# Kernel optimization log

Hardware: AMD Instinct MI355X
Metric: run time of the kernel (lower is better)

The kernel has to match this reference:

```python
import jax, jax.numpy as jnp
import numpy as np

N, C, D = 200000, 100, 256      # samples, classes, dim_out
M = N // C                       # samples per class (y is sorted, equal counts)
K = int(1000 * 0.1)              # num_overlab = int(args.d * args.overlap_ratio)
ALPHA = 1.0                      # args.alpha


def setup_inputs() -> dict:
    key = jax.random.key(0)
    x = jax.random.normal(key, (N, D), dtype=jnp.float32)
    # sorted, balanced labels: class c occupies rows [c*M, (c+1)*M)
    y = jnp.arange(N, dtype=jnp.int32) // M
    return {"x": x, "y": y}


def reference(x, y):
    # per-class means (faithful to get_centers); y is sorted/balanced so a
    # reshape gives the static per-class grouping used below
    xg = x.reshape(C, M, D)                         # [C, M, D]
    centers = jax.ops.segment_sum(x, y, num_segments=C) / M  # [C, D]

    # full center-to-sample L2 distances via ||c||^2 + ||x||^2 - 2 c.x
    x2 = jnp.sum(xg * xg, axis=-1)                  # [C2, M]
    c2 = jnp.sum(centers * centers, axis=-1)        # [C1]
    cx = jnp.einsum('cd,gmd->cgm', centers, xg)     # [C1, C2, M]
    dist = jnp.sqrt(jnp.maximum(c2[:, None, None] + x2[None, :, :] - 2.0 * cx, 0.0))

    # positive: K largest distances from each center to its own samples
    pos = jnp.einsum('iim->im', dist)               # diagonal blocks [C, M]
    pos_mean = jax.lax.top_k(pos, K)[0].mean(axis=1)            # [C]

    # negative: K smallest distances from center c1 to samples of class c2
    neg_mean = (-jax.lax.top_k(-dist, K)[0]).mean(axis=-1)      # [C1, C2]

    lo = jnp.maximum(ALPHA + pos_mean[:, None] - neg_mean, 0.0)  # [C1, C2]
    mask = 1.0 - jnp.eye(C, dtype=lo.dtype)         # skip class_type2 == class_type1
    loss = jnp.sum(lo * mask) / ((C + 1) * (C / 2))
    return loss.reshape(1)
```

## Files before the change

### kernel.cpp

```cpp
#include <hip/hip_runtime.h>
#include <hip/hip_fp16.h>
#include <math.h>

#define N_S 200000
#define C_CLS 100
#define D_DIM 256
#define M_PER 2000
#define K_SEL 100
#define EP_STRIDE 136

typedef __attribute__((ext_vector_type(8))) short short8;
typedef __attribute__((ext_vector_type(4))) float float4v;

__device__ __forceinline__ unsigned int f2bf(float f){
    unsigned int u = __float_as_uint(f);
    u += 0x7FFFu + ((u >> 16) & 1u);
    return u >> 16;
}

__global__ __launch_bounds__(256) void k_sums(const float* __restrict__ x,
                                              float* __restrict__ partial){
    int c = blockIdx.x, s = blockIdx.y;
    int t = threadIdx.x, w = t >> 6, ch = t & 63;
    int rbase = c * M_PER + s * 125;
    float a0 = 0.f, a1 = 0.f, a2 = 0.f, a3 = 0.f;
    for (int i = 0; i < 32; ++i){
        int rl = w + 4 * i;
        if (rl < 125){
            float4v v = *(const float4v*)(x + (size_t)(rbase + rl) * D_DIM + ch * 4);
            a0 += v[0]; a1 += v[1]; a2 += v[2]; a3 += v[3];
        }
    }
    float4v o = {a0, a1, a2, a3};
    *(float4v*)(partial + ((size_t)((c * 16 + s) * 4 + w)) * D_DIM + ch * 4) = o;
}

__global__ __launch_bounds__(256) void k_centers(const float* __restrict__ partial,
                                                 unsigned short* __restrict__ cbf,
                                                 float* __restrict__ c2){
    int c = blockIdx.x, d = threadIdx.x;
    const float* pp = partial + (size_t)c * 64 * D_DIM + d;
    float v = 0.f;
    #pragma unroll
    for (int s = 0; s < 64; ++s) v += pp[(size_t)s * D_DIM];
    v *= (1.0f / (float)M_PER);
    cbf[c * D_DIM + d] = (unsigned short)f2bf(v);
    float sq = v * v;
    #pragma unroll
    for (int m = 1; m < 64; m <<= 1) sq += __shfl_xor(sq, m);
    __shared__ float sred[4];
    if ((threadIdx.x & 63) == 0) sred[threadIdx.x >> 6] = sq;
    __syncthreads();
    if (threadIdx.x == 0) c2[c] = (sred[0] + sred[1]) + (sred[2] + sred[3]);
}

__global__ __launch_bounds__(256, 3) void k_gemm(const float* __restrict__ x,
                                                 const unsigned short* __restrict__ cbf,
                                                 const float* __restrict__ c2,
                                                 _Float16* __restrict__ dist2h){
    __shared__ unsigned short s_cent[C_CLS * 264];
    __shared__ float s_c2[C_CLS];
    int tid = threadIdx.x;
    {
        const uint4* g = (const uint4*)cbf;
        #pragma unroll
        for (int i = 0; i < 13; ++i){
            int q = i * 256 + tid;
            if (q < 3200){
                uint4 v = g[q];
                int row = q >> 5;
                int col = q & 31;
                *(uint4*)((char*)s_cent + row * 528 + col * 16) = v;
            }
        }
        if (tid < C_CLS) s_c2[tid] = c2[tid];
    }
    __syncthreads();

    int wid = tid >> 6, lane = tid & 63, lo = lane & 15, hi = lane >> 4;
    int sbase = blockIdx.x * 128 + wid * 32;
    int j0 = sbase + lo, j1 = sbase + 16 + lo;
    int jr0 = j0 < N_S ? j0 : N_S - 1;
    int jr1 = j1 < N_S ? j1 : N_S - 1;

    float4v acc[7][2];
    #pragma unroll
    for (int a = 0; a < 7; ++a){
        #pragma unroll
        for (int b = 0; b < 2; ++b) acc[a][b] = (float4v){0.f, 0.f, 0.f, 0.f};
    }
    float px2_0 = 0.f, px2_1 = 0.f;

    const float* xr0 = x + (size_t)jr0 * D_DIM + hi * 8;
    const float* xr1 = x + (size_t)jr1 * D_DIM + hi * 8;
    for (int ks = 0; ks < 8; ++ks){
        int k0 = ks * 32;
        float4v v0 = *(const float4v*)(xr0 + k0);
        float4v v1 = *(const float4v*)(xr0 + k0 + 4);
        float4v w0 = *(const float4v*)(xr1 + k0);
        float4v w1 = *(const float4v*)(xr1 + k0 + 4);
        px2_0 += v0[0]*v0[0] + v0[1]*v0[1] + v0[2]*v0[2] + v0[3]*v0[3]
               + v1[0]*v1[0] + v1[1]*v1[1] + v1[2]*v1[2] + v1[3]*v1[3];
        px2_1 += w0[0]*w0[0] + w0[1]*w0[1] + w0[2]*w0[2] + w0[3]*w0[3]
               + w1[0]*w1[0] + w1[1]*w1[1] + w1[2]*w1[2] + w1[3]*w1[3];
        short8 bfr0, bfr1;
        bfr0[0]=(short)f2bf(v0[0]); bfr0[1]=(short)f2bf(v0[1]); bfr0[2]=(short)f2bf(v0[2]); bfr0[3]=(short)f2bf(v0[3]);
        bfr0[4]=(short)f2bf(v1[0]); bfr0[5]=(short)f2bf(v1[1]); bfr0[6]=(short)f2bf(v1[2]); bfr0[7]=(short)f2bf(v1[3]);
        bfr1[0]=(short)f2bf(w0[0]); bfr1[1]=(short)f2bf(w0[1]); bfr1[2]=(short)f2bf(w0[2]); bfr1[3]=(short)f2bf(w0[3]);
        bfr1[4]=(short)f2bf(w1[0]); bfr1[5]=(short)f2bf(w1[1]); bfr1[6]=(short)f2bf(w1[2]); bfr1[7]=(short)f2bf(w1[3]);
        #pragma unroll
        for (int cf = 0; cf < 7; ++cf){
            short8 afr = *(const short8*)((const char*)s_cent + (cf*16 + lo) * 528 + (k0 + hi*8) * 2);
            acc[cf][0] = __builtin_amdgcn_mfma_f32_16x16x32_bf16(afr, bfr0, acc[cf][0], 0, 0, 0);
            acc[cf][1] = __builtin_amdgcn_mfma_f32_16x16x32_bf16(afr, bfr1, acc[cf][1], 0, 0, 0);
        }
    }

    px2_0 += __shfl_xor(px2_0, 16); px2_0 += __shfl_xor(px2_0, 32);
    px2_1 += __shfl_xor(px2_1, 16); px2_1 += __shfl_xor(px2_1, 32);

    __syncthreads();
    _Float16* ep = (_Float16*)s_cent;
    #pragma unroll
    for (int sf = 0; sf < 2; ++sf){
        float x2 = sf ? px2_1 : px2_0;
        int lj = wid * 32 + sf * 16 + lo;
        #pragma unroll
        for (int cf = 0; cf < 7; ++cf){
            #pragma unroll
            for (int r = 0; r < 4; ++r){
                int c1 = cf * 16 + hi * 4 + r;
                if (c1 < C_CLS){
                    float d2 = s_c2[c1] + x2 - 2.0f * acc[cf][sf][r];
                    ep[c1 * EP_STRIDE + lj] = (_Float16)fmaxf(d2, 0.f);
                }
            }
        }
    }
    __syncthreads();

    int blockbase = blockIdx.x * 128;
    int vj = N_S - blockbase; vj = vj > 128 ? 128 : vj;
    for (int q = tid; q < C_CLS * 16; q += 256){
        int row = q >> 4, st = (q & 15) * 8;
        if (st < vj){
            uint4 v = *(const uint4*)(ep + row * EP_STRIDE + st);
            *(uint4*)(dist2h + (size_t)row * N_S + blockbase + st) = v;
        }
    }
}

__global__ __launch_bounds__(256) void k_select(const _Float16* __restrict__ dist2h,
                                                float* __restrict__ pos_mean,
                                                float* __restrict__ neg_mean){
    int lane = threadIdx.x & 63;
    int pair = blockIdx.x * 4 + (threadIdx.x >> 6);
    int c1 = pair / 100, c2 = pair - c1 * 100;
    bool diag = (c1 == c2);
    const uint4* base =
        (const uint4*)(dist2h + (size_t)c1 * N_S + (size_t)c2 * M_PER);

    unsigned pk[16];
    int kmin = 0x10000, kmax = 0;
    #pragma unroll
    for (int i = 0; i < 4; ++i){
        int q = i * 64 + lane;
        uint4 v;
        if (q < 250){
            v = base[q];
            if (diag){ v.x = ~v.x; v.y = ~v.y; v.z = ~v.z; v.w = ~v.w; }
            unsigned wds[4] = {v.x, v.y, v.z, v.w};
            #pragma unroll
            for (int j = 0; j < 4; ++j){
                int a = (int)(wds[j] & 0xFFFFu);
                int b = (int)(wds[j] >> 16);
                kmin = a < kmin ? a : kmin;  kmin = b < kmin ? b : kmin;
                kmax = a > kmax ? a : kmax;  kmax = b > kmax ? b : kmax;
            }
        } else {
            v.x = v.y = v.z = v.w = 0xFFFFFFFFu;
        }
        pk[i*4 + 0] = v.x; pk[i*4 + 1] = v.y; pk[i*4 + 2] = v.z; pk[i*4 + 3] = v.w;
    }
    #pragma unroll
    for (int m = 1; m < 64; m <<= 1){
        int a = __shfl_xor(kmin, m); kmin = a < kmin ? a : kmin;
        int b = __shfl_xor(kmax, m); kmax = b > kmax ? b : kmax;
    }

    int lo = kmin, hi = kmax;
    while (lo < hi){
        int mid = (lo + hi) >> 1;
        int c = 0;
        #pragma unroll
        for (int i = 0; i < 16; ++i){
            c += (int)__popcll(__ballot((int)(pk[i] & 0xFFFFu) <= mid));
            c += (int)__popcll(__ballot((int)(pk[i] >> 16)     <= mid));
        }
        if (c >= K_SEL) hi = mid; else lo = mid + 1;
    }
    int t = lo;

    float sb = 0.f;
    int nb = 0;
    #pragma unroll
    for (int i = 0; i < 16; ++i){
        int ka = (int)(pk[i] & 0xFFFFu);
        int kb = (int)(pk[i] >> 16);
        if (ka < t){
            unsigned short u = (unsigned short)(diag ? (0xFFFF - ka) : ka);
            sb += sqrtf(__half2float(__ushort_as_half(u)));
        }
        if (kb < t){
            unsigned short u = (unsigned short)(diag ? (0xFFFF - kb) : kb);
            sb += sqrtf(__half2float(__ushort_as_half(u)));
        }
        nb += (int)__popcll(__ballot(ka < t));
        nb += (int)__popcll(__ballot(kb < t));
    }
    #pragma unroll
    for (int m = 1; m < 64; m <<= 1) sb += __shfl_xor(sb, m);

    if (lane == 0){
        unsigned short ut = (unsigned short)(diag ? (0xFFFF - t) : t);
        float tval = sqrtf(__half2float(__ushort_as_half(ut)));
        int need = K_SEL - nb;
        float mean = (sb + (float)need * tval) * (1.0f / (float)K_SEL);
        if (diag) pos_mean[c1] = mean; else neg_mean[pair] = mean;
    }
}

__global__ __launch_bounds__(256) void k_loss(const float* __restrict__ pos_mean,
                                              const float* __restrict__ neg_mean,
                                              float* __restrict__ out){
    __shared__ float sred[4];
    int tid = threadIdx.x;
    float s = 0.f;
    for (int idx = tid; idx < C_CLS * C_CLS; idx += 256){
        int c1 = idx / 100, c2 = idx - c1 * 100;
        if (c1 != c2){
            float v = 1.0f + pos_mean[c1] - neg_mean[idx];
            s += fmaxf(v, 0.f);
        }
    }
    #pragma unroll
    for (int m = 1; m < 64; m <<= 1) s += __shfl_xor(s, m);
    if ((tid & 63) == 0) sred[tid >> 6] = s;
    __syncthreads();
    if (tid == 0) out[0] = ((sred[0] + sred[1]) + (sred[2] + sred[3])) * (1.0f / 5050.0f);
}

extern "C" void kernel_launch(void* const* d_in, const int* in_sizes, int n_in,
                              void* d_out, int out_size, void* d_ws, size_t ws_size,
                              hipStream_t stream){
    const float* x = (const float*)d_in[0];
    char* ws = (char*)d_ws;
    _Float16*       dist2h   = (_Float16*)(ws);
    float*          partial  = (float*)(ws + 40000000);
    unsigned short* cbf      = (unsigned short*)(ws + 46553600);
    float*          c2       = (float*)(ws + 46604800);
    float*          pos_mean = (float*)(ws + 46605200);
    float*          neg_mean = (float*)(ws + 46605600);
    float* out = (float*)d_out;

    hipLaunchKernelGGL(k_sums,    dim3(100, 16), dim3(256), 0, stream, x, partial);
    hipLaunchKernelGGL(k_centers, dim3(C_CLS),   dim3(256), 0, stream, partial, cbf, c2);
    hipLaunchKernelGGL(k_gemm,    dim3(1563),    dim3(256), 0, stream, x, cbf, c2, dist2h);
    hipLaunchKernelGGL(k_select,  dim3(2500),    dim3(256), 0, stream, dist2h, pos_mean, neg_mean);
    hipLaunchKernelGGL(k_loss,    dim3(1),       dim3(256), 0, stream, pos_mean, neg_mean, out);
}
```

Before: 126.7 us.

## Fuse all stages into one persistent cooperative kernel with grid syncs

Replaces the five separate launches (sums, centers, gemm, select, loss) with a single cooperative persistent kernel that loops over each stage's tiles and uses grid-wide syncs between stages. This is meant to remove per-launch overhead and the tail gaps between kernels. In exchange, the grid is capped at two blocks per CU, so large stages like the GEMM and selection lose some parallelism. The kernel also makes extra host queries (device attribute, occupancy) on every call, and falls back to the old launches if the cooperative launch fails.

```diff
diff --git a/kernel.cpp b/kernel.cpp
--- a/kernel.cpp
+++ b/kernel.cpp
@@ -1,6 +1,9 @@
 #include <hip/hip_runtime.h>
+#include <hip/hip_cooperative_groups.h>
 #include <hip/hip_fp16.h>
 #include <math.h>
+
+namespace cg = cooperative_groups;
 
 #define N_S 200000
 #define C_CLS 100
@@ -8,6 +11,7 @@
 #define M_PER 2000
 #define K_SEL 100
 #define EP_STRIDE 136
+#define NUM_CU 256
 
 typedef __attribute__((ext_vector_type(8))) short short8;
 typedef __attribute__((ext_vector_type(4))) float float4v;
@@ -16,6 +20,243 @@
     unsigned int u = __float_as_uint(f);
     u += 0x7FFFu + ((u >> 16) & 1u);
     return u >> 16;
+}
+
+__global__ __launch_bounds__(256, 2) void k_fused(const float* __restrict__ x,
+                                                  float* __restrict__ partial,
+                                                  unsigned short* __restrict__ cbf,
+                                                  float* __restrict__ c2,
+                                                  _Float16* __restrict__ dist2h,
+                                                  float* __restrict__ pos_mean,
+                                                  float* __restrict__ neg_mean,
+                                                  float* __restrict__ out){
+    cg::grid_group grid = cg::this_grid();
+    __shared__ unsigned short s_cent[C_CLS * 264];
+    __shared__ float s_c2[C_CLS];
+    __shared__ float sred[4];
+
+    int tid = threadIdx.x;
+    int wid = tid >> 6, lane = tid & 63;
+
+    for (int t = blockIdx.x; t < 1600; t += gridDim.x){
+        int c = t >> 4, s = t & 15;
+        int rbase = c * M_PER + s * 125;
+        float a0 = 0.f, a1 = 0.f, a2 = 0.f, a3 = 0.f;
+        for (int i = 0; i < 32; ++i){
+            int rl = wid + 4 * i;
+            if (rl < 125){
+                float4v v = *(const float4v*)(x + (size_t)(rbase + rl) * D_DIM + lane * 4);
+                a0 += v[0]; a1 += v[1]; a2 += v[2]; a3 += v[3];
+            }
+        }
+        float4v o = {a0, a1, a2, a3};
+        *(float4v*)(partial + ((size_t)((c * 16 + s) * 4 + wid)) * D_DIM + lane * 4) = o;
+    }
+    grid.sync();
+
+    for (int c = blockIdx.x; c < C_CLS; c += gridDim.x){
+        __syncthreads();
+        int d = tid;
+        const float* pp = partial + (size_t)c * 64 * D_DIM + d;
+        float v = 0.f;
+        #pragma unroll
+        for (int s = 0; s < 64; ++s) v += pp[(size_t)s * D_DIM];
+        v *= (1.0f / (float)M_PER);
+        cbf[c * D_DIM + d] = (unsigned short)f2bf(v);
+        float sq = v * v;
+        #pragma unroll
+        for (int m = 1; m < 64; m <<= 1) sq += __shfl_xor(sq, m);
+        if (lane == 0) sred[wid] = sq;
+        __syncthreads();
+        if (tid == 0) c2[c] = (sred[0] + sred[1]) + (sred[2] + sred[3]);
+    }
+    grid.sync();
+
+    for (int t = blockIdx.x; t < 1563; t += gridDim.x){
+        __syncthreads();
+        {
+            const uint4* g = (const uint4*)cbf;
+            #pragma unroll
+            for (int i = 0; i < 13; ++i){
+                int q = i * 256 + tid;
+                if (q < 3200){
+                    uint4 v = g[q];
+                    int row = q >> 5;
+                    int col = q & 31;
+                    *(uint4*)((char*)s_cent + row * 528 + col * 16) = v;
+                }
+            }
+            if (tid < C_CLS) s_c2[tid] = c2[tid];
+        }
+        __syncthreads();
+
+        int lo = lane & 15, hi = lane >> 4;
+        int sbase = t * 128 + wid * 32;
+        int j0 = sbase + lo, j1 = sbase + 16 + lo;
+        int jr0 = j0 < N_S ? j0 : N_S - 1;
+        int jr1 = j1 < N_S ? j1 : N_S - 1;
+
+        float4v acc[7][2];
+        #pragma unroll
+        for (int a = 0; a < 7; ++a){
+            #pragma unroll
+            for (int b = 0; b < 2; ++b) acc[a][b] = (float4v){0.f, 0.f, 0.f, 0.f};
+        }
+        float px2_0 = 0.f, px2_1 = 0.f;
+
+        const float* xr0 = x + (size_t)jr0 * D_DIM + hi * 8;
+        const float* xr1 = x + (size_t)jr1 * D_DIM + hi * 8;
+        for (int ks = 0; ks < 8; ++ks){
+            int k0 = ks * 32;
+            float4v v0 = *(const float4v*)(xr0 + k0);
+            float4v v1 = *(const float4v*)(xr0 + k0 + 4);
+            float4v w0 = *(const float4v*)(xr1 + k0);
+            float4v w1 = *(const float4v*)(xr1 + k0 + 4);
+            px2_0 += v0[0]*v0[0] + v0[1]*v0[1] + v0[2]*v0[2] + v0[3]*v0[3]
+                   + v1[0]*v1[0] + v1[1]*v1[1] + v1[2]*v1[2] + v1[3]*v1[3];
+            px2_1 += w0[0]*w0[0] + w0[1]*w0[1] + w0[2]*w0[2] + w0[3]*w0[3]
+                   + w1[0]*w1[0] + w1[1]*w1[1] + w1[2]*w1[2] + w1[3]*w1[3];
+            short8 bfr0, bfr1;
+            bfr0[0]=(short)f2bf(v0[0]); bfr0[1]=(short)f2bf(v0[1]); bfr0[2]=(short)f2bf(v0[2]); bfr0[3]=(short)f2bf(v0[3]);
+            bfr0[4]=(short)f2bf(v1[0]); bfr0[5]=(short)f2bf(v1[1]); bfr0[6]=(short)f2bf(v1[2]); bfr0[7]=(short)f2bf(v1[3]);
+            bfr1[0]=(short)f2bf(w0[0]); bfr1[1]=(short)f2bf(w0[1]); bfr1[2]=(short)f2bf(w0[2]); bfr1[3]=(short)f2bf(w0[3]);
+            bfr1[4]=(short)f2bf(w1[0]); bfr1[5]=(short)f2bf(w1[1]); bfr1[6]=(short)f2bf(w1[2]); bfr1[7]=(short)f2bf(w1[3]);
+            #pragma unroll
+            for (int cf = 0; cf < 7; ++cf){
+                short8 afr = *(const short8*)((const char*)s_cent + (cf*16 + lo) * 528 + (k0 + hi*8) * 2);
+                acc[cf][0] = __builtin_amdgcn_mfma_f32_16x16x32_bf16(afr, bfr0, acc[cf][0], 0, 0, 0);
+                acc[cf][1] = __builtin_amdgcn_mfma_f32_16x16x32_bf16(afr, bfr1, acc[cf][1], 0, 0, 0);
+            }
+        }
+
+        px2_0 += __shfl_xor(px2_0, 16); px2_0 += __shfl_xor(px2_0, 32);
+        px2_1 += __shfl_xor(px2_1, 16); px2_1 += __shfl_xor(px2_1, 32);
+
+        __syncthreads();
+        _Float16* ep = (_Float16*)s_cent;
+        #pragma unroll
+        for (int sf = 0; sf < 2; ++sf){
+            float x2 = sf ? px2_1 : px2_0;
+            int lj = wid * 32 + sf * 16 + lo;
+            #pragma unroll
+            for (int cf = 0; cf < 7; ++cf){
+                #pragma unroll
+                for (int r = 0; r < 4; ++r){
+                    int c1 = cf * 16 + hi * 4 + r;
+                    if (c1 < C_CLS){
+                        float d2 = s_c2[c1] + x2 - 2.0f * acc[cf][sf][r];
+                        ep[c1 * EP_STRIDE + lj] = (_Float16)fmaxf(d2, 0.f);
+                    }
+                }
+            }
+        }
+        __syncthreads();
+
+        int blockbase = t * 128;
+        int vj = N_S - blockbase; vj = vj > 128 ? 128 : vj;
+        for (int q = tid; q < C_CLS * 16; q += 256){
+            int row = q >> 4, st = (q & 15) * 8;
+            if (st < vj){
+                uint4 v = *(const uint4*)(ep + row * EP_STRIDE + st);
+                *(uint4*)(dist2h + (size_t)row * N_S + blockbase + st) = v;
+            }
+        }
+    }
+    grid.sync();
+
+    for (int task = blockIdx.x; task < 2500; task += gridDim.x){
+        int pair = task * 4 + wid;
+        int c1 = pair / 100, c2i = pair - c1 * 100;
+        bool diag = (c1 == c2i);
+        const uint4* base =
+            (const uint4*)(dist2h + (size_t)c1 * N_S + (size_t)c2i * M_PER);
+
+        unsigned pk[16];
+        int kmin = 0x10000, kmax = 0;
+        #pragma unroll
+        for (int i = 0; i < 4; ++i){
+            int q = i * 64 + lane;
+            uint4 v;
+            if (q < 250){
+                v = base[q];
+                if (diag){ v.x = ~v.x; v.y = ~v.y; v.z = ~v.z; v.w = ~v.w; }
+                unsigned wds[4] = {v.x, v.y, v.z, v.w};
+                #pragma unroll
+                for (int j = 0; j < 4; ++j){
+                    int a = (int)(wds[j] & 0xFFFFu);
+                    int b = (int)(wds[j] >> 16);
+                    kmin = a < kmin ? a : kmin;  kmin = b < kmin ? b : kmin;
+                    kmax = a > kmax ? a : kmax;  kmax = b > kmax ? b : kmax;
+                }
+            } else {
+                v.x = v.y = v.z = v.w = 0xFFFFFFFFu;
+            }
+            pk[i*4 + 0] = v.x; pk[i*4 + 1] = v.y; pk[i*4 + 2] = v.z; pk[i*4 + 3] = v.w;
+        }
+        #pragma unroll
+        for (int m = 1; m < 64; m <<= 1){
+            int a = __shfl_xor(kmin, m); kmin = a < kmin ? a : kmin;
+            int b = __shfl_xor(kmax, m); kmax = b > kmax ? b : kmax;
+        }
+
+        int lo = kmin, hi = kmax;
+        while (lo < hi){
+            int mid = (lo + hi) >> 1;
+            int c = 0;
+            #pragma unroll
+            for (int i = 0; i < 16; ++i){
+                c += (int)__popcll(__ballot((int)(pk[i] & 0xFFFFu) <= mid));
+                c += (int)__popcll(__ballot((int)(pk[i] >> 16)     <= mid));
+            }
+            if (c >= K_SEL) hi = mid; else lo = mid + 1;
+        }
+        int th = lo;
+
+        float sb = 0.f;
+        int nb = 0;
+        #pragma unroll
+        for (int i = 0; i < 16; ++i){
+            int ka = (int)(pk[i] & 0xFFFFu);
+            int kb = (int)(pk[i] >> 16);
+            if (ka < th){
+                unsigned short u = (unsigned short)(diag ? (0xFFFF - ka) : ka);
+                sb += sqrtf(__half2float(__ushort_as_half(u)));
+            }
+            if (kb < th){
+                unsigned short u = (unsigned short)(diag ? (0xFFFF - kb) : kb);
+                sb += sqrtf(__half2float(__ushort_as_half(u)));
+            }
+            nb += (int)__popcll(__ballot(ka < th));
+            nb += (int)__popcll(__ballot(kb < th));
+        }
+        #pragma unroll
+        for (int m = 1; m < 64; m <<= 1) sb += __shfl_xor(sb, m);
+
+        if (lane == 0){
+            unsigned short ut = (unsigned short)(diag ? (0xFFFF - th) : th);
+            float tval = sqrtf(__half2float(__ushort_as_half(ut)));
+            int need = K_SEL - nb;
+            float mean = (sb + (float)need * tval) * (1.0f / (float)K_SEL);
+            if (diag) pos_mean[c1] = mean; else neg_mean[pair] = mean;
+        }
+    }
+    grid.sync();
+
+    if (blockIdx.x == 0){
+        float s = 0.f;
+        for (int idx = tid; idx < C_CLS * C_CLS; idx += 256){
+            int a = idx / 100, b = idx - a * 100;
+            if (a != b){
+                float v = 1.0f + pos_mean[a] - neg_mean[idx];
+                s += fmaxf(v, 0.f);
+            }
+        }
+        #pragma unroll
+        for (int m = 1; m < 64; m <<= 1) s += __shfl_xor(s, m);
+        if (lane == 0) sred[wid] = s;
+        __syncthreads();
+        if (tid == 0) out[0] = ((sred[0] + sred[1]) + (sred[2] + sred[3])) * (1.0f / 5050.0f);
+    }
 }
 
 __global__ __launch_bounds__(256) void k_sums(const float* __restrict__ x,
@@ -261,11 +502,30 @@
     float*          c2       = (float*)(ws + 46604800);
     float*          pos_mean = (float*)(ws + 46605200);
     float*          neg_mean = (float*)(ws + 46605600);
-    float* out = (float*)d_out;
-
-    hipLaunchKernelGGL(k_sums,    dim3(100, 16), dim3(256), 0, stream, x, partial);
-    hipLaunchKernelGGL(k_centers, dim3(C_CLS),   dim3(256), 0, stream, partial, cbf, c2);
-    hipLaunchKernelGGL(k_gemm,    dim3(1563),    dim3(256), 0, stream, x, cbf, c2, dist2h);
-    hipLaunchKernelGGL(k_select,  dim3(2500),    dim3(256), 0, stream, dist2h, pos_mean, neg_mean);
-    hipLaunchKernelGGL(k_loss,    dim3(1),       dim3(256), 0, stream, pos_mean, neg_mean, out);
-}
+    float*          out      = (float*)d_out;
+
+    int dev = 0;
+    (void)hipGetDevice(&dev);
+    int coop = 0;
+    (void)hipDeviceGetAttribute(&coop, hipDeviceAttributeCooperativeLaunch, dev);
+    int maxB = 0;
+    (void)hipOccupancyMaxActiveBlocksPerMultiprocessor(&maxB, (const void*)k_fused, 256, 0);
+
+    bool launched = false;
+    if (coop && maxB >= 1){
+        int bpc = maxB < 2 ? maxB : 2;
+        dim3 grid((unsigned)(bpc * NUM_CU));
+        void* args[] = {(void*)&x, (void*)&partial, (void*)&cbf, (void*)&c2,
+                        (void*)&dist2h, (void*)&pos_mean, (void*)&neg_mean, (void*)&out};
+        hipError_t e = hipLaunchCooperativeKernel((const void*)k_fused, grid, dim3(256),
+                                                  args, 0, stream);
+        launched = (e == hipSuccess);
+    }
+    if (!launched){
+        hipLaunchKernelGGL(k_sums,    dim3(100, 16), dim3(256), 0, stream, x, partial);
+        hipLaunchKernelGGL(k_centers, dim3(C_CLS),   dim3(256), 0, stream, partial, cbf, c2);
+        hipLaunchKernelGGL(k_gemm,    dim3(1563),    dim3(256), 0, stream, x, cbf, c2, dist2h);
+        hipLaunchKernelGGL(k_select,  dim3(2500),    dim3(256), 0, stream, dist2h, pos_mean, neg_mean);
+        hipLaunchKernelGGL(k_loss,    dim3(1),       dim3(256), 0, stream, pos_mean, neg_mean, out);
+    }
+}
```

New measurement: 322.2 us. 154% more time.
